# Optimization experiments

Hardware: AMD Instinct MI355X
Metric: run time of the kernel (lower is better)

Reference implementation:

```python
import jax, jax.numpy as jnp
import numpy as np

D_MODEL = 1024
NUM_HEADS = 16
QUERY_GROUPS = 4
HEAD_DIM = D_MODEL // NUM_HEADS  # 64
HPG = NUM_HEADS // QUERY_GROUPS  # heads per group = 4
SCALE = 0.125  # softmax_scale = 1/sqrt(head_dim)

B, T_FRAMES, HW, T_TOKENS = 2, 16, 1024, 77


def setup_inputs() -> dict:
    key = jax.random.key(0)
    ks = jax.random.split(key, 8)
    s = 0.02
    return {
        "x": jax.random.normal(ks[0], (B, T_FRAMES, HW, D_MODEL), jnp.float32),
        "text_embeddings": jax.random.normal(ks[1], (B, T_TOKENS, D_MODEL), jnp.float32),
        "padding_mask": jnp.ones((B, T_TOKENS), dtype=bool),  # True = attend
        "use_mqa": 0,
        "use_qk_norm": 0,
        "Wq": jax.random.normal(ks[2], (D_MODEL, NUM_HEADS * HEAD_DIM), jnp.float32) * s,
        "Wk": jax.random.normal(ks[3], (D_MODEL, QUERY_GROUPS * HEAD_DIM), jnp.float32) * s,
        "Wv": jax.random.normal(ks[4], (D_MODEL, QUERY_GROUPS * HEAD_DIM), jnp.float32) * s,
        "Wo": jax.random.normal(ks[5], (D_MODEL, D_MODEL), jnp.float32) * s,
        "Wst": jax.random.normal(ks[6], (2 * D_MODEL, D_MODEL), jnp.float32) * s,
    }


def _attend(q, k, v, mask):
    """q: [B, R, H, Lq, hd]; k, v: [B, H, Tt, hd]; mask: [B, Tt] bool.

    The torch module repeat_interleaves k/v (and the mask) over the R axis
    before SDPA; broadcasting over R computes identical math without the copy.
    """
    scores = jnp.einsum('brhqd,bhkd->brhqk', q, k) * SCALE
    neg = jnp.asarray(jnp.finfo(scores.dtype).min, scores.dtype)
    scores = jnp.where(mask[:, None, None, None, :], scores, neg)
    p = jax.nn.softmax(scores, axis=-1)
    return jnp.einsum('brhqk,bhkd->brhqd', p, v)


def reference(x, text_embeddings, padding_mask, use_mqa, use_qk_norm, Wq, Wk, Wv, Wo, Wst):
    b, t, hw, _ = x.shape
    tt = text_embeddings.shape[1]
    # shared GQA key/value projections, expanded from query_groups to num_heads
    k = (text_embeddings @ Wk).reshape(b, tt, QUERY_GROUPS, HEAD_DIM)
    v = (text_embeddings @ Wv).reshape(b, tt, QUERY_GROUPS, HEAD_DIM)
    k = jnp.repeat(k, HPG, axis=2).transpose(0, 2, 1, 3)  # [B, H, Tt, hd]
    v = jnp.repeat(v, HPG, axis=2).transpose(0, 2, 1, 3)

    # spatial branch: queries are spatial patches, independent per frame
    qs = (x @ Wq).reshape(b, t, hw, NUM_HEADS, HEAD_DIM).transpose(0, 1, 3, 2, 4)  # [B,T,H,HW,hd]
    spatial = _attend(qs, k, v, padding_mask)
    spatial = spatial.transpose(0, 1, 3, 2, 4).reshape(b, t, hw, D_MODEL)

    # temporal branch: queries are frames, independent per spatial patch
    xt = x.transpose(0, 2, 1, 3)  # [B, HW, T, d]
    qt = (xt @ Wq).reshape(b, hw, t, NUM_HEADS, HEAD_DIM).transpose(0, 1, 3, 2, 4)  # [B,HW,H,T,hd]
    temporal = _attend(qt, k, v, padding_mask)
    temporal = temporal.transpose(0, 1, 3, 2, 4).reshape(b, hw, t, D_MODEL).transpose(0, 2, 1, 3)

    fused = jnp.concatenate([spatial, temporal], axis=-1) @ Wst  # [B,T,HW,d]
    return fused @ Wo
```

## Files before the change

### kernel.cpp

```cpp
#include <hip/hip_runtime.h>

typedef unsigned short u16;
typedef __attribute__((ext_vector_type(8))) short short8;
typedef __attribute__((ext_vector_type(4))) float f32x4;

__device__ __forceinline__ u16 f2bf(float f) {
    unsigned u = __builtin_bit_cast(unsigned, f);
    u += 0x7FFFu + ((u >> 16) & 1u);
    return (u16)(u >> 16);
}
__device__ __forceinline__ float bf2f(u16 h) {
    unsigned u = ((unsigned)h) << 16;
    return __builtin_bit_cast(float, u);
}

#define GLD_LDS(g, l) \
    __builtin_amdgcn_global_load_lds((const __attribute__((address_space(1))) void*)(g), \
                                     (__attribute__((address_space(3))) void*)(l), 16, 0, 0)

#define WAITV(n) asm volatile("s_waitcnt vmcnt(" #n ")" ::: "memory")
#define BARM()                                  \
    do {                                        \
        asm volatile("" ::: "memory");          \
        __builtin_amdgcn_s_barrier();           \
        asm volatile("" ::: "memory");          \
    } while (0)

__device__ __forceinline__ void xcd_swizzle(int& bx, int& by) {
    const int nwg = gridDim.x * gridDim.y;
    const int flat = blockIdx.y * gridDim.x + blockIdx.x;
    const int cpx = nwg >> 3;
    const int nf = (flat & 7) * cpx + (flat >> 3);
    bx = nf % gridDim.x;
    by = nf / gridDim.x;
}

__global__ void sniff_dtype(const u16* __restrict__ wq, int* __restrict__ flag) {
    __shared__ int cnt;
    if (threadIdx.x == 0) cnt = 0;
    __syncthreads();
    int local = 0;
    for (int i = threadIdx.x; i < 1024; i += 256) {
        const int e = (wq[i] >> 7) & 0xFF;
        if (e >= 0x81) local++;
    }
    atomicAdd(&cnt, local);
    __syncthreads();
    if (threadIdx.x == 0) *flag = (cnt >= 32) ? 1 : 0;
}

__global__ void cvt_copy8(const void* __restrict__ in, long off,
                          u16* __restrict__ out, long n,
                          const int* __restrict__ flag) {
    const long stride = (long)gridDim.x * 256 * 8;
    long i = ((long)blockIdx.x * 256 + threadIdx.x) * 8;
    if (*flag) {
        const float* p = (const float*)in + off;
        for (; i < n; i += stride) {
            const f32x4 a = *(const f32x4*)(p + i);
            const f32x4 b = *(const f32x4*)(p + i + 4);
            short8 h;
#pragma unroll
            for (int j = 0; j < 4; j++) {
                h[j] = (short)f2bf(a[j]);
                h[j + 4] = (short)f2bf(b[j]);
            }
            *(short8*)(out + i) = h;
        }
    } else {
        const u16* p = (const u16*)in + off;
        for (; i < n; i += stride) *(short8*)(out + i) = *(const short8*)(p + i);
    }
}

__global__ void transpose_cvt(const void* __restrict__ in, u16* __restrict__ out,
                              const int* __restrict__ flag) {
    __shared__ u16 t[32][33];
    const int x0 = blockIdx.x * 32, y0 = blockIdx.y * 32;
    const int tx = threadIdx.x, ty = threadIdx.y;
    if (*flag) {
        const float* p = (const float*)in;
        for (int dy = ty; dy < 32; dy += 8)
            t[dy][tx] = f2bf(p[(size_t)(y0 + dy) * 1024 + x0 + tx]);
    } else {
        const u16* p = (const u16*)in;
        for (int dy = ty; dy < 32; dy += 8)
            t[dy][tx] = p[(size_t)(y0 + dy) * 1024 + x0 + tx];
    }
    __syncthreads();
    for (int dy = ty; dy < 32; dy += 8)
        out[(size_t)(x0 + dy) * 1024 + y0 + tx] = t[tx][dy];
}

__global__ void transpose_kv(const void* __restrict__ in, u16* __restrict__ out,
                             const int* __restrict__ flag) {
    __shared__ u16 t[32][33];
    const int x0 = blockIdx.x * 32, y0 = blockIdx.y * 32;
    const int tx = threadIdx.x, ty = threadIdx.y;
    if (*flag) {
        const float* p = (const float*)in;
        for (int dy = ty; dy < 32; dy += 8)
            t[dy][tx] = f2bf(p[(size_t)(y0 + dy) * 256 + x0 + tx]);
    } else {
        const u16* p = (const u16*)in;
        for (int dy = ty; dy < 32; dy += 8)
            t[dy][tx] = p[(size_t)(y0 + dy) * 256 + x0 + tx];
    }
    __syncthreads();
    for (int dy = ty; dy < 32; dy += 8)
        out[(size_t)(x0 + dy) * 1024 + y0 + tx] = t[tx][dy];
}

__global__ void cvt_pad_text(const void* __restrict__ in, u16* __restrict__ out,
                             const int* __restrict__ flag) {
    const int row = blockIdx.x, b = row >> 7, t = row & 127;
    const int j = threadIdx.x * 8;
    short8 h = {0, 0, 0, 0, 0, 0, 0, 0};
    if (t < 77) {
        if (*flag) {
            const float* p = (const float*)in + ((size_t)(b * 77 + t)) * 1024 + j;
            const f32x4 a = *(const f32x4*)p;
            const f32x4 c = *(const f32x4*)(p + 4);
#pragma unroll
            for (int k = 0; k < 4; k++) {
                h[k] = (short)f2bf(a[k]);
                h[k + 4] = (short)f2bf(c[k]);
            }
        } else {
            h = *(const short8*)((const u16*)in + ((size_t)(b * 77 + t)) * 1024 + j);
        }
    }
    *(short8*)&out[(size_t)row * 1024 + j] = h;
}

__global__ void repack_kv(const u16* __restrict__ Kall, u16* __restrict__ Kp,
                          u16* __restrict__ VT) {
    const int g = blockIdx.x, b = blockIdx.y;
    const int tid = threadIdx.x;
    for (int idx = tid; idx < 80 * 64; idx += 256) {
        const int tok = idx >> 6, d = idx & 63;
        Kp[((size_t)(b * 4 + g) * 80 + tok) * 64 + d] =
            Kall[(size_t)(b * 128 + tok) * 512 + g * 64 + d];
    }
    for (int idx = tid; idx < 64 * 96; idx += 256) {
        const int d = idx / 96, tok = idx - d * 96;
        VT[(size_t)(b * 4 + g) * 6144 + d * 96 + tok] =
            Kall[(size_t)(b * 128 + tok) * 512 + 256 + g * 64 + d];
    }
}

__global__ void gemm_bt(const u16* __restrict__ A, const u16* __restrict__ BT,
                        u16* __restrict__ C, int K, int lda, int ldb, int ldc) {
    __shared__ __align__(16) u16 As[512 * 8];
    __shared__ __align__(16) u16 Bs[512 * 8];
    const int tid = threadIdx.x;
    const int wave = tid >> 6, lane = tid & 63, quad = lane >> 4, r = lane & 15;
    const int wm = (wave >> 1) * 64, wn = (wave & 1) * 64;
    int bx, by;
    xcd_swizzle(bx, by);
    const long m0 = (long)by * 128, n0 = (long)bx * 128;

    f32x4 acc[4][4] = {};
    const int c0 = wave * 64 + lane, c1 = (wave + 4) * 64 + lane;
    const int kc0 = c0 >> 7, mm0 = c0 & 127, kc1 = c1 >> 7, mm1 = c1 & 127;
    const u16* ga0 = A + (m0 + mm0) * (long)lda + kc0 * 8;
    const u16* ga1 = A + (m0 + mm1) * (long)lda + kc1 * 8;
    const u16* gb0 = BT + (n0 + mm0) * (long)ldb + kc0 * 8;
    const u16* gb1 = BT + (n0 + mm1) * (long)ldb + kc1 * 8;

    for (int k0 = 0; k0 < K; k0 += 32) {
        GLD_LDS(ga0 + k0, &As[wave * 64 * 8]);
        GLD_LDS(ga1 + k0, &As[(wave + 4) * 64 * 8]);
        GLD_LDS(gb0 + k0, &Bs[wave * 64 * 8]);
        GLD_LDS(gb1 + k0, &Bs[(wave + 4) * 64 * 8]);
        __syncthreads();
        short8 af[4], bfr[4];
#pragma unroll
        for (int mt = 0; mt < 4; mt++)
            af[mt] = *(const short8*)&As[(quad * 128 + wm + mt * 16 + r) * 8];
#pragma unroll
        for (int nt = 0; nt < 4; nt++)
            bfr[nt] = *(const short8*)&Bs[(quad * 128 + wn + nt * 16 + r) * 8];
#pragma unroll
        for (int mt = 0; mt < 4; mt++)
#pragma unroll
            for (int nt = 0; nt < 4; nt++)
                acc[mt][nt] = __builtin_amdgcn_mfma_f32_16x16x32_bf16(
                    af[mt], bfr[nt], acc[mt][nt], 0, 0, 0);
        __syncthreads();
    }
#pragma unroll
    for (int mt = 0; mt < 4; mt++)
#pragma unroll
        for (int nt = 0; nt < 4; nt++)
#pragma unroll
            for (int reg = 0; reg < 4; reg++) {
                const long row = m0 + wm + mt * 16 + quad * 4 + reg;
                const long col = n0 + wn + nt * 16 + r;
                C[row * (long)ldc + col] = f2bf(acc[mt][nt][reg]);
            }
}

__device__ __forceinline__ void stage_ht(const u16* __restrict__ src, long ld,
                                         u16* lds, int half, int wave, int lane) {
#pragma unroll
    for (int j = 0; j < 2; j++) {
        const int idx0 = j * 512 + wave * 64;
        const int kc = idx0 >> 7, ml0 = idx0 & 127;
        GLD_LDS(src + (long)(half * 128 + ml0 + lane) * ld + kc * 8,
                lds + (kc * 256 + half * 128 + ml0) * 8);
    }
}

template <int MODE>
__global__ __launch_bounds__(512, 2) void gemm256(
    const u16* __restrict__ A1, const u16* __restrict__ A2,
    const u16* __restrict__ BT, void* __restrict__ outv, long base,
    const int* __restrict__ flag) {
    __shared__ __align__(16) u16 As[2][8 * 256 * 8];
    __shared__ __align__(16) u16 Bs[2][8 * 256 * 8];
    const int tid = threadIdx.x;
    const int wave = tid >> 6, lane = tid & 63, quad = lane >> 4, r = lane & 15;
    const int wr = wave >> 2, wc = wave & 3;
    int bx, by;
    xcd_swizzle(bx, by);
    const long m0 = (long)by * 256, n0 = (long)bx * 256;
    const int ldb = MODE ? 2048 : 1024;
    const int NT = MODE ? 32 : 16;

    f32x4 acc[8][4] = {};

    auto asrc = [&](int tt) -> const u16* {
        if (MODE == 0) return A1 + m0 * 1024 + (long)tt * 64;
        return (tt < 16) ? (A1 + m0 * 1024 + (long)tt * 64)
                         : (A2 + m0 * 1024 + (long)(tt - 16) * 64);
    };
    const u16* bbase = BT + n0 * (long)ldb;

    stage_ht(asrc(0), 1024, As[0], 0, wave, lane);
    stage_ht(asrc(0), 1024, As[0], 1, wave, lane);
    stage_ht(bbase, ldb, Bs[0], 0, wave, lane);
    stage_ht(bbase, ldb, Bs[0], 1, wave, lane);

#define QUADX(mb)                                                              \
    {                                                                          \
        short8 afx[2][2];                                                      \
        _Pragma("unroll") for (int mi = 0; mi < 2; mi++)                       \
            _Pragma("unroll") for (int ks = 0; ks < 2; ks++)                   \
                afx[mi][ks] = *(const short8*)&As[c][((ks * 4 + quad) * 256 +  \
                    wr * 128 + (mb + mi) * 16 + r) * 8];                       \
        __builtin_amdgcn_s_setprio(1);                                         \
        _Pragma("unroll") for (int mi = 0; mi < 2; mi++)                       \
            _Pragma("unroll") for (int nt = 0; nt < 4; nt++)                   \
                _Pragma("unroll") for (int ks = 0; ks < 2; ks++)               \
                    acc[mb + mi][nt] = __builtin_amdgcn_mfma_f32_16x16x32_bf16(\
                        afx[mi][ks], bf[nt][ks], acc[mb + mi][nt], 0, 0, 0);   \
        __builtin_amdgcn_s_setprio(0);                                         \
    }

#pragma unroll 2
    for (int t = 0; t < NT; t++) {
        const int c = t & 1, n = c ^ 1;
        const bool have = (t + 1 < NT);
        const u16* an = asrc(t + 1 < NT ? t + 1 : t);
        const u16* bn = bbase + (long)(t + 1) * 64;
        if (have) {
            stage_ht(an, 1024, As[n], 0, wave, lane);
            WAITV(2);
        } else {
            WAITV(0);
        }
        BARM();
        short8 bf[4][2];
#pragma unroll
        for (int nt = 0; nt < 4; nt++)
#pragma unroll
            for (int ks = 0; ks < 2; ks++)
                bf[nt][ks] = *(const short8*)&Bs[c][((ks * 4 + quad) * 256 +
                                                     wc * 64 + nt * 16 + r) * 8];
        QUADX(0);
        if (have) stage_ht(an, 1024, As[n], 1, wave, lane);
        QUADX(2);
        if (have) stage_ht(bn, ldb, Bs[n], 0, wave, lane);
        QUADX(4);
        if (have) stage_ht(bn, ldb, Bs[n], 1, wave, lane);
        QUADX(6);
        BARM();
    }
#undef QUADX

    if (MODE == 0) {
        u16* o = (u16*)outv;
#pragma unroll
        for (int mt = 0; mt < 8; mt++)
#pragma unroll
            for (int nt = 0; nt < 4; nt++)
#pragma unroll
                for (int reg = 0; reg < 4; reg++)
                    o[(m0 + wr * 128 + mt * 16 + quad * 4 + reg) * 1024L + n0 +
                      wc * 64 + nt * 16 + r] = f2bf(acc[mt][nt][reg]);
    } else if (*flag) {
        float* o = (float*)outv + base;
#pragma unroll
        for (int mt = 0; mt < 8; mt++)
#pragma unroll
            for (int nt = 0; nt < 4; nt++)
#pragma unroll
                for (int reg = 0; reg < 4; reg++)
                    o[(m0 + wr * 128 + mt * 16 + quad * 4 + reg) * 1024L + n0 +
                      wc * 64 + nt * 16 + r] = acc[mt][nt][reg];
    } else {
        u16* o = (u16*)outv + base;
#pragma unroll
        for (int mt = 0; mt < 8; mt++)
#pragma unroll
            for (int nt = 0; nt < 4; nt++)
#pragma unroll
                for (int reg = 0; reg < 4; reg++)
                    o[(m0 + wr * 128 + mt * 16 + quad * 4 + reg) * 1024L + n0 +
                      wc * 64 + nt * 16 + r] = f2bf(acc[mt][nt][reg]);
    }
}

__device__ __forceinline__ void attn_core(const short8 aq0, const short8 aq1,
                                          const u16* Kl, const u16* Vl, u16* Plw,
                                          const int quad, const int r, f32x4 o[4]) {
    f32x4 sc[5];
#pragma unroll
    for (int nt = 0; nt < 5; nt++) {
        f32x4 z = {0.f, 0.f, 0.f, 0.f};
        const short8 bk0 = *(const short8*)&Kl[(nt * 16 + r) * 72 + quad * 8];
        const short8 bk1 = *(const short8*)&Kl[(nt * 16 + r) * 72 + 32 + quad * 8];
        z = __builtin_amdgcn_mfma_f32_16x16x32_bf16(aq0, bk0, z, 0, 0, 0);
        z = __builtin_amdgcn_mfma_f32_16x16x32_bf16(aq1, bk1, z, 0, 0, 0);
        sc[nt] = z;
    }
#pragma unroll
    for (int reg = 0; reg < 4; reg++) {
        float v[5];
        float mx = -3e38f;
#pragma unroll
        for (int nt = 0; nt < 5; nt++) {
            float s = sc[nt][reg] * 0.125f;
            if (nt == 4 && r >= 13) s = -3e38f;
            v[nt] = s;
            mx = fmaxf(mx, s);
        }
#pragma unroll
        for (int off = 1; off < 16; off <<= 1) mx = fmaxf(mx, __shfl_xor(mx, off));
        float sum = 0.f;
#pragma unroll
        for (int nt = 0; nt < 5; nt++) {
            v[nt] = __expf(v[nt] - mx);
            sum += v[nt];
        }
#pragma unroll
        for (int off = 1; off < 16; off <<= 1) sum += __shfl_xor(sum, off);
        const float inv = 1.0f / sum;
#pragma unroll
        for (int nt = 0; nt < 5; nt++)
            Plw[(quad * 4 + reg) * 104 + nt * 16 + r] = f2bf(v[nt] * inv);
    }
    __syncthreads();
    const short8 ap0 = *(const short8*)&Plw[r * 104 + quad * 8];
    const short8 ap1 = *(const short8*)&Plw[r * 104 + 32 + quad * 8];
    const short8 ap2 = *(const short8*)&Plw[r * 104 + 64 + quad * 8];
#pragma unroll
    for (int nt = 0; nt < 4; nt++) {
        f32x4 z = {0.f, 0.f, 0.f, 0.f};
        const short8 bv0 = *(const short8*)&Vl[(nt * 16 + r) * 104 + quad * 8];
        const short8 bv1 = *(const short8*)&Vl[(nt * 16 + r) * 104 + 32 + quad * 8];
        const short8 bv2 = *(const short8*)&Vl[(nt * 16 + r) * 104 + 64 + quad * 8];
        z = __builtin_amdgcn_mfma_f32_16x16x32_bf16(ap0, bv0, z, 0, 0, 0);
        z = __builtin_amdgcn_mfma_f32_16x16x32_bf16(ap1, bv1, z, 0, 0, 0);
        z = __builtin_amdgcn_mfma_f32_16x16x32_bf16(ap2, bv2, z, 0, 0, 0);
        o[nt] = z;
    }
}

__global__ void attn_spatial(const u16* __restrict__ Q, const u16* __restrict__ Kp,
                             const u16* __restrict__ VT, u16* __restrict__ S) {
    const int qc = blockIdx.x, h = blockIdx.y, t = blockIdx.z;
    const int g = h >> 2;
    __shared__ __align__(16) u16 Kl[80 * 72];
    __shared__ __align__(16) u16 Vl[64 * 104];
    __shared__ __align__(16) u16 Pl[4][16 * 104];
    const int tid = threadIdx.x;
    const int wave = tid >> 6, lane = tid & 63, quad = lane >> 4, r = lane & 15;

    const u16* Kg = Kp + (size_t)g * 80 * 64;
    for (int idx = tid; idx < 80 * 64; idx += 256)
        Kl[(idx >> 6) * 72 + (idx & 63)] = Kg[idx];
    const u16* Vg = VT + (size_t)g * 64 * 96;
    for (int idx = tid; idx < 64 * 96; idx += 256) {
        const int d = idx / 96, tk = idx - d * 96;
        Vl[d * 104 + tk] = Vg[idx];
    }
#pragma unroll
    for (int j = 0; j < 4; j++) Pl[wave][r * 104 + 80 + quad * 4 + j] = 0;
    __syncthreads();

    const size_t qrow = (size_t)t * 1024 + qc * 64 + wave * 16 + r;
    const u16* Qb = Q + qrow * 1024 + h * 64;
    const short8 aq0 = *(const short8*)(Qb + quad * 8);
    const short8 aq1 = *(const short8*)(Qb + 32 + quad * 8);

    f32x4 o[4];
    attn_core(aq0, aq1, Kl, Vl, Pl[wave], quad, r, o);

    const size_t srow0 = (size_t)t * 1024 + qc * 64 + wave * 16 + quad * 4;
#pragma unroll
    for (int nt = 0; nt < 4; nt++)
#pragma unroll
        for (int reg = 0; reg < 4; reg++)
            S[(srow0 + reg) * 1024 + h * 64 + nt * 16 + r] = f2bf(o[nt][reg]);
}

__global__ void attn_temporal(u16* Q, const u16* __restrict__ Kp,
                              const u16* __restrict__ VT) {
    const int hw0 = blockIdx.x * 4, h = blockIdx.y;
    const int g = h >> 2;
    __shared__ __align__(16) u16 Kl[80 * 72];
    __shared__ __align__(16) u16 Vl[64 * 104];
    __shared__ __align__(16) u16 Ql[4][16 * 72];
    __shared__ __align__(16) u16 Pl[4][16 * 104];
    const int tid = threadIdx.x;
    const int wave = tid >> 6, lane = tid & 63, quad = lane >> 4, r = lane & 15;

    const u16* Kg = Kp + (size_t)g * 80 * 64;
    for (int idx = tid; idx < 80 * 64; idx += 256)
        Kl[(idx >> 6) * 72 + (idx & 63)] = Kg[idx];
    const u16* Vg = VT + (size_t)g * 64 * 96;
    for (int idx = tid; idx < 64 * 96; idx += 256) {
        const int d = idx / 96, tk = idx - d * 96;
        Vl[d * 104 + tk] = Vg[idx];
    }
    for (int idx = tid; idx < 4096; idx += 256) {
        const int hwl = idx >> 10, t = (idx >> 6) & 15, d = idx & 63;
        Ql[hwl][t * 72 + d] = Q[((size_t)t * 1024 + hw0 + hwl) * 1024 + h * 64 + d];
    }
#pragma unroll
    for (int j = 0; j < 4; j++) Pl[wave][r * 104 + 80 + quad * 4 + j] = 0;
    __syncthreads();

    const short8 aq0 = *(const short8*)&Ql[wave][r * 72 + quad * 8];
    const short8 aq1 = *(const short8*)&Ql[wave][r * 72 + 32 + quad * 8];

    f32x4 o[4];
    attn_core(aq0, aq1, Kl, Vl, Pl[wave], quad, r, o);

    const int hw = hw0 + wave;
#pragma unroll
    for (int nt = 0; nt < 4; nt++)
#pragma unroll
        for (int reg = 0; reg < 4; reg++)
            Q[((size_t)(quad * 4 + reg) * 1024 + hw) * 1024 + h * 64 + nt * 16 + r] =
                f2bf(o[nt][reg]);
}

extern "C" void kernel_launch(void* const* d_in, const int* in_sizes, int n_in,
                              void* d_out, int out_size, void* d_ws, size_t ws_size,
                              hipStream_t stream) {
    const void* x    = d_in[0];
    const void* text = d_in[1];
    const void* Wq   = d_in[5];
    const void* Wk   = d_in[6];
    const void* Wv   = d_in[7];
    const void* Wo   = d_in[8];
    const void* Wst  = d_in[9];
    char* ws = (char*)d_ws;

    int* flag  = (int*)(ws);
    u16* WqT   = (u16*)(ws + 64);
    u16* WoT   = (u16*)(ws + 2097216);
    u16* Wstc  = (u16*)(ws + 4194368);
    u16* W12T  = (u16*)(ws + 8388672);
    u16* Kp    = (u16*)(ws + 12898368);
    u16* VTb   = (u16*)(ws + 12980288);
    u16* Qws   = (u16*)(ws + 13078592);
    u16* Sws   = (u16*)(ws + 46633024);
    u16* textp = Sws;
    u16* WkvT  = (u16*)(ws + 46633024 + 524288);
    u16* Kall  = (u16*)(ws + 46633024 + 1572864);

    sniff_dtype<<<1, 256, 0, stream>>>((const u16*)Wq, flag);
    cvt_copy8<<<1024, 256, 0, stream>>>(Wst, 0, Wstc, 2097152L, flag);
    transpose_cvt<<<dim3(32, 32), dim3(32, 8), 0, stream>>>(Wq, WqT, flag);
    transpose_cvt<<<dim3(32, 32), dim3(32, 8), 0, stream>>>(Wo, WoT, flag);
    gemm_bt<<<dim3(16, 8), 256, 0, stream>>>(WoT, Wstc, W12T, 1024, 1024, 1024, 2048);

    transpose_kv<<<dim3(8, 32), dim3(32, 8), 0, stream>>>(Wk, WkvT, flag);
    transpose_kv<<<dim3(8, 32), dim3(32, 8), 0, stream>>>(Wv, WkvT + 256 * 1024, flag);
    cvt_pad_text<<<256, 128, 0, stream>>>(text, textp, flag);
    gemm_bt<<<dim3(4, 2), 256, 0, stream>>>(textp, WkvT, Kall, 1024, 1024, 1024, 512);
    repack_kv<<<dim3(4, 2), 256, 0, stream>>>(Kall, Kp, VTb);

    for (int b = 0; b < 2; b++) {
        const long xbase = (long)b * 16777216;
        const u16* Kpb = Kp + (size_t)b * 20480;
        const u16* VTp = VTb + (size_t)b * 24576;

        cvt_copy8<<<2048, 256, 0, stream>>>(x, xbase, Sws, 16777216L, flag);
        gemm256<0><<<dim3(4, 64), 512, 0, stream>>>(Sws, nullptr, WqT, Qws, 0, flag);
        attn_spatial<<<dim3(16, 16, 16), 256, 0, stream>>>(Qws, Kpb, VTp, Sws);
        attn_temporal<<<dim3(256, 16), 256, 0, stream>>>(Qws, Kpb, VTp);
        gemm256<1><<<dim3(4, 64), 512, 0, stream>>>(Sws, Qws, W12T, d_out, xbase, flag);
    }
}
```

Before: 782.5 us.

## Stage GEMM tiles by K-half and split main loop into two barrier phases

Global-to-LDS staging now splits each 256x64 tile along K into two halves instead of along M rows. The main loop becomes two phases, each synchronized on only its K-half being resident. This lets compute on the first K-half begin while the second half's loads are still in flight. It adds a barrier per iteration and reorders the vmcnt waits, with some risk of extra sync stalls.

```diff
diff --git a/kernel.cpp b/kernel.cpp
--- a/kernel.cpp
+++ b/kernel.cpp
@@ -201,15 +201,16 @@
             }
 }
 
-__device__ __forceinline__ void stage_ht(const u16* __restrict__ src, long ld,
-                                         u16* lds, int half, int wave, int lane) {
+__device__ __forceinline__ void stage_kh(const u16* __restrict__ src, long ld,
+                                         u16* lds, int kh, int wave, int lane) {
 #pragma unroll
     for (int j = 0; j < 2; j++) {
         const int idx0 = j * 512 + wave * 64;
-        const int kc = idx0 >> 7, ml0 = idx0 & 127;
-        GLD_LDS(src + (long)(half * 128 + ml0 + lane) * ld + kc * 8,
-                lds + (kc * 256 + half * 128 + ml0) * 8);
-    }
+        const int kc = kh * 4 + (idx0 >> 8), row0 = idx0 & 255;
+        GLD_LDS(src + (long)(row0 + lane) * ld + kc * 8,
+                lds + (kh * 1024 + idx0) * 8);
+    }
+    asm volatile("" ::: "memory");
 }
 
 template <int MODE>
@@ -237,57 +238,65 @@
     };
     const u16* bbase = BT + n0 * (long)ldb;
 
-    stage_ht(asrc(0), 1024, As[0], 0, wave, lane);
-    stage_ht(asrc(0), 1024, As[0], 1, wave, lane);
-    stage_ht(bbase, ldb, Bs[0], 0, wave, lane);
-    stage_ht(bbase, ldb, Bs[0], 1, wave, lane);
-
-#define QUADX(mb)                                                              \
-    {                                                                          \
-        short8 afx[2][2];                                                      \
-        _Pragma("unroll") for (int mi = 0; mi < 2; mi++)                       \
-            _Pragma("unroll") for (int ks = 0; ks < 2; ks++)                   \
-                afx[mi][ks] = *(const short8*)&As[c][((ks * 4 + quad) * 256 +  \
-                    wr * 128 + (mb + mi) * 16 + r) * 8];                       \
-        __builtin_amdgcn_s_setprio(1);                                         \
-        _Pragma("unroll") for (int mi = 0; mi < 2; mi++)                       \
-            _Pragma("unroll") for (int nt = 0; nt < 4; nt++)                   \
-                _Pragma("unroll") for (int ks = 0; ks < 2; ks++)               \
-                    acc[mb + mi][nt] = __builtin_amdgcn_mfma_f32_16x16x32_bf16(\
-                        afx[mi][ks], bf[nt][ks], acc[mb + mi][nt], 0, 0, 0);   \
-        __builtin_amdgcn_s_setprio(0);                                         \
-    }
+    stage_kh(asrc(0), 1024, As[0], 0, wave, lane);
+    stage_kh(bbase, ldb, Bs[0], 0, wave, lane);
+    stage_kh(asrc(0), 1024, As[0], 1, wave, lane);
+    stage_kh(bbase, ldb, Bs[0], 1, wave, lane);
+
+#define PH_READ_B(kh)                                                         \
+    _Pragma("unroll") for (int nt = 0; nt < 4; nt++)                          \
+        bf[nt] = *(const short8*)&Bs[c][(((kh) * 4 + quad) * 256 +            \
+                                         wc * 64 + nt * 16 + r) * 8];
+#define PH_READ_A(kh, mb0)                                                    \
+    _Pragma("unroll") for (int mi = 0; mi < 4; mi++)                          \
+        afx[mi] = *(const short8*)&As[c][(((kh) * 4 + quad) * 256 +           \
+                                          wr * 128 + ((mb0) + mi) * 16 + r) * 8];
+#define PH_MFMA(mb0)                                                          \
+    __builtin_amdgcn_s_setprio(1);                                            \
+    _Pragma("unroll") for (int mi = 0; mi < 4; mi++)                          \
+        _Pragma("unroll") for (int nt = 0; nt < 4; nt++)                      \
+            acc[(mb0) + mi][nt] = __builtin_amdgcn_mfma_f32_16x16x32_bf16(    \
+                afx[mi], bf[nt], acc[(mb0) + mi][nt], 0, 0, 0);               \
+    __builtin_amdgcn_s_setprio(0);
 
 #pragma unroll 2
     for (int t = 0; t < NT; t++) {
         const int c = t & 1, n = c ^ 1;
         const bool have = (t + 1 < NT);
-        const u16* an = asrc(t + 1 < NT ? t + 1 : t);
+        const u16* an = asrc(have ? t + 1 : t);
         const u16* bn = bbase + (long)(t + 1) * 64;
+        short8 bf[4], afx[4];
         if (have) {
-            stage_ht(an, 1024, As[n], 0, wave, lane);
-            WAITV(2);
+            stage_kh(an, 1024, As[n], 0, wave, lane);
+            WAITV(6);
+        } else {
+            WAITV(4);
+        }
+        BARM();
+        PH_READ_B(0);
+        PH_READ_A(0, 0);
+        PH_MFMA(0);
+        PH_READ_A(0, 4);
+        if (have) stage_kh(bn, ldb, Bs[n], 0, wave, lane);
+        PH_MFMA(4);
+        if (have) {
+            stage_kh(an, 1024, As[n], 1, wave, lane);
+            WAITV(6);
         } else {
             WAITV(0);
         }
         BARM();
-        short8 bf[4][2];
-#pragma unroll
-        for (int nt = 0; nt < 4; nt++)
-#pragma unroll
-            for (int ks = 0; ks < 2; ks++)
-                bf[nt][ks] = *(const short8*)&Bs[c][((ks * 4 + quad) * 256 +
-                                                     wc * 64 + nt * 16 + r) * 8];
-        QUADX(0);
-        if (have) stage_ht(an, 1024, As[n], 1, wave, lane);
-        QUADX(2);
-        if (have) stage_ht(bn, ldb, Bs[n], 0, wave, lane);
-        QUADX(4);
-        if (have) stage_ht(bn, ldb, Bs[n], 1, wave, lane);
-        QUADX(6);
+        PH_READ_B(1);
+        PH_READ_A(1, 0);
+        PH_MFMA(0);
+        PH_READ_A(1, 4);
+        if (have) stage_kh(bn, ldb, Bs[n], 1, wave, lane);
+        PH_MFMA(4);
         BARM();
     }
-#undef QUADX
+#undef PH_READ_B
+#undef PH_READ_A
+#undef PH_MFMA
 
     if (MODE == 0) {
         u16* o = (u16*)outv;
```

Result: faster. 739.9 us (-5.4%).
